# Performance work log

Measured on AMD Instinct MI355X. Metric: run time of the kernel, lower is better.

The kernel has to match this reference:

```python
import jax, jax.numpy as jnp
import numpy as np

B, S, H, NH, L, MLP_MULT = 4, 1024, 1024, 16, 2, 4
DK = H // NH
EPS = 1e-5


def setup_inputs() -> dict:
    key = jax.random.key(0)
    ks = jax.random.split(key, 8)
    p = lambda k, shape: jax.random.normal(k, shape, dtype=jnp.float32) * 0.02
    return {
        'hidden_states': jax.random.normal(ks[0], (B, S, H), dtype=jnp.float32),
        'attn_w': p(ks[1], (L, H, 3 * H)),
        'attn_b': jnp.zeros((L, 3 * H), jnp.float32),
        'proj_w': p(ks[2], (L, H, H)),
        'proj_b': jnp.zeros((L, H), jnp.float32),
        'fc_w': p(ks[3], (L, H, MLP_MULT * H)),
        'fc_b': jnp.zeros((L, MLP_MULT * H), jnp.float32),
        'fc2_w': p(ks[4], (L, MLP_MULT * H, H)),
        'fc2_b': jnp.zeros((L, H), jnp.float32),
        'ln1_g': jnp.ones((L, H), jnp.float32),
        'ln1_b': jnp.zeros((L, H), jnp.float32),
        'ln2_g': jnp.ones((L, H), jnp.float32),
        'ln2_b': jnp.zeros((L, H), jnp.float32),
        'position_ids': jnp.arange(S, dtype=jnp.int32),
    }


def _ln(x, g, b):
    m = jnp.mean(x, axis=-1, keepdims=True)
    v = jnp.var(x, axis=-1, keepdims=True)
    return (x - m) * jax.lax.rsqrt(v + EPS) * g + b


def _rotate_half(x):
    x1, x2 = jnp.split(x, 2, axis=-1)
    return jnp.concatenate((-x2, x1), axis=-1)


def _forward(hidden_states, attn_w, attn_b, proj_w, proj_b, fc_w, fc_b,
             fc2_w, fc2_b, ln1_g, ln1_b, ln2_g, ln2_b, position_ids):
    # rotary tables (fp32 math, as in RotaryEmbedding.forward)
    inv_freq = 1.0 / (10000.0 ** (jnp.arange(0, DK, 2, dtype=jnp.float32) / DK))
    freqs = position_ids.astype(jnp.float32)[:, None] * inv_freq[None, :]  # [S, DK/2]
    emb = jnp.concatenate((freqs, freqs), axis=-1)                          # [S, DK]
    cos = jnp.cos(emb)[None, None]  # [1,1,S,DK]
    sin = jnp.sin(emb)[None, None]
    causal = jnp.tril(jnp.ones((S, S), dtype=bool))
    neg = jnp.finfo(jnp.float32).min
    scale = 1.0 / np.sqrt(DK).astype(np.float32)

    h = hidden_states
    for i in range(L):
        # attention block
        x = _ln(h, ln1_g[i], ln1_b[i])
        qkv = x @ attn_w[i] + attn_b[i]                  # Conv1D c_attn
        q, k, v = jnp.split(qkv, 3, axis=-1)
        heads = lambda t: t.reshape(B, S, NH, DK).transpose(0, 2, 1, 3)
        q, k, v = heads(q), heads(k), heads(v)           # [B,NH,S,DK]
        q = q * cos + _rotate_half(q) * sin
        k = k * cos + _rotate_half(k) * sin
        # fp32 QK^T (baddbmm with alpha=scale, beta=0)
        w = jnp.einsum('bhqd,bhkd->bhqk', q.astype(jnp.float32),
                       k.astype(jnp.float32)) * scale    # [B,NH,S,S]
        w = jnp.where(causal, w, neg)
        w = jax.nn.softmax(w, axis=-1).astype(v.dtype)   # attn dropout is identity (eval)
        a = jnp.einsum('bhqk,bhkd->bhqd', w, v)
        a = a.transpose(0, 2, 1, 3).reshape(B, S, H)     # merge_heads
        h = h + (a @ proj_w[i] + proj_b[i])              # c_proj + residual
        # MLP block (gelu_new == tanh-approx gelu)
        x = _ln(h, ln2_g[i], ln2_b[i])
        mid = jax.nn.gelu(x @ fc_w[i] + fc_b[i], approximate=True)
        h = h + (mid @ fc2_w[i] + fc2_b[i])
    return h


def reference(hidden_states, attn_w, attn_b, proj_w, proj_b, fc_w, fc_b,
              fc2_w, fc2_b, ln1_g, ln1_b, ln2_g, ln2_b, position_ids):
    return _forward(hidden_states, attn_w, attn_b, proj_w, proj_b, fc_w, fc_b,
                    fc2_w, fc2_b, ln1_g, ln1_b, ln2_g, ln2_b, position_ids)
```

## Files before the change

kernel.cpp:

```cpp
#include <hip/hip_runtime.h>

#define B_ 4
#define S_ 1024
#define H_ 1024
#define NH_ 16
#define DK_ 64
#define MLPH_ 4096
#define EPS_ 1e-5f

typedef __attribute__((ext_vector_type(8))) short short8_t;
typedef __attribute__((ext_vector_type(8))) unsigned short ushort8_t;
typedef __attribute__((ext_vector_type(4))) float f32x4;

__device__ __forceinline__ unsigned short f2bf(float f) {
  unsigned int u = __float_as_uint(f);
  u = u + 0x7fffu + ((u >> 16) & 1u);
  return (unsigned short)(u >> 16);
}
__device__ __forceinline__ float bf2f(unsigned short b) {
  return __uint_as_float(((unsigned int)b) << 16);
}

__device__ __forceinline__ void gload16(const void* g, void* l) {
  typedef const __attribute__((address_space(1))) unsigned int GU;
  typedef __attribute__((address_space(3))) unsigned int LU;
  __builtin_amdgcn_global_load_lds((GU*)(size_t)g, (LU*)(unsigned int)(size_t)l, 16, 0, 0);
}

__device__ __forceinline__ float gelu_tanh(float x) {
  float y = 1.5957691216057308f * (x + 0.044715f * x * x * x);
  return x / (1.0f + __expf(-y));
}

__global__ __launch_bounds__(256) void wconv(const float* __restrict__ src0,
                                             unsigned short* __restrict__ dst0,
                                             int K, int N) {
  __shared__ float t[32][33];
  const float* src = src0 + (size_t)blockIdx.z * K * N;
  unsigned short* dst = dst0 + (size_t)blockIdx.z * N * K;
  int n0 = blockIdx.x * 32, k0 = blockIdx.y * 32;
  int tid = threadIdx.x;
  int r = tid >> 3, c = (tid & 7) * 4;
  const float* s = src + (size_t)(k0 + r) * N + n0 + c;
  float4 v = *(const float4*)s;
  t[r][c] = v.x; t[r][c + 1] = v.y; t[r][c + 2] = v.z; t[r][c + 3] = v.w;
  __syncthreads();
  ushort4 o;
  o.x = f2bf(t[c + 0][r]); o.y = f2bf(t[c + 1][r]);
  o.z = f2bf(t[c + 2][r]); o.w = f2bf(t[c + 3][r]);
  *(ushort4*)(dst + (size_t)(n0 + r) * K + k0 + c) = o;
}

__global__ __launch_bounds__(256) void ln_kernel(const float* __restrict__ x,
                                                 const float* __restrict__ g,
                                                 const float* __restrict__ b,
                                                 unsigned short* __restrict__ y) {
  int row = blockIdx.x, tid = threadIdx.x;
  const float* xp = x + (size_t)row * H_;
  float4 v = *((const float4*)xp + tid);
  float s  = v.x + v.y + v.z + v.w;
  float s2 = v.x * v.x + v.y * v.y + v.z * v.z + v.w * v.w;
  #pragma unroll
  for (int o = 1; o < 64; o <<= 1) {
    s  += __shfl_xor(s, o, 64);
    s2 += __shfl_xor(s2, o, 64);
  }
  __shared__ float r1[4], r2[4];
  if ((tid & 63) == 0) { r1[tid >> 6] = s; r2[tid >> 6] = s2; }
  __syncthreads();
  s  = r1[0] + r1[1] + r1[2] + r1[3];
  s2 = r2[0] + r2[1] + r2[2] + r2[3];
  float mean = s * (1.0f / H_);
  float var  = s2 * (1.0f / H_) - mean * mean;
  float inv  = rsqrtf(var + EPS_);
  float4 gv = *((const float4*)g + tid);
  float4 bv = *((const float4*)b + tid);
  ushort4 o;
  o.x = f2bf((v.x - mean) * inv * gv.x + bv.x);
  o.y = f2bf((v.y - mean) * inv * gv.y + bv.y);
  o.z = f2bf((v.z - mean) * inv * gv.z + bv.z);
  o.w = f2bf((v.w - mean) * inv * gv.w + bv.w);
  *(ushort4*)(y + (size_t)row * H_ + tid * 4) = o;
}

template <int MODE, int NT>
__global__ __launch_bounds__(256) void gemm_mfma(
    const unsigned short* __restrict__ A, const unsigned short* __restrict__ Bt,
    const float* __restrict__ bias, const float* __restrict__ resid,
    void* __restrict__ outp, int M, int N, int K, const int* __restrict__ pos) {
  constexpr int BN = NT * 32;
  constexpr int CB = BN / 32;
  __shared__ __align__(16) unsigned short As[2][128 * 64];
  __shared__ __align__(16) unsigned short Bs[2][BN * 64];
  int tid = threadIdx.x;
  int w = tid >> 6, lane = tid & 63;
  int gx = gridDim.x;
  int nwg = gx * gridDim.y;
  int bid = blockIdx.y * gx + blockIdx.x;
  int cpx = nwg >> 3;
  int swz = (bid & 7) * cpx + (bid >> 3);
  int m0 = (swz / gx) * 128, n0 = (swz % gx) * BN;
  int wr = w >> 1, wc = w & 1;
  int fr = lane & 15, kg = lane >> 4;
  f32x4 acc[4][NT];
  #pragma unroll
  for (int m = 0; m < 4; m++)
    #pragma unroll
    for (int n = 0; n < NT; n++) {
      acc[m][n][0] = 0.f; acc[m][n][1] = 0.f; acc[m][n][2] = 0.f; acc[m][n][3] = 0.f;
    }
  int srow = lane >> 3;
  int scol = ((lane & 7) ^ srow) * 8;
  const unsigned short* Ap = A  + (size_t)(m0 + w * 32 + srow) * K + scol;
  const unsigned short* Bp = Bt + (size_t)(n0 + w * (8 * CB) + srow) * K + scol;
  int sx = (fr & 7);
  int nk = K >> 6;
  {
    char* AsB = (char*)As[0] + w * 4096;
    char* BsB = (char*)Bs[0] + w * CB * 1024;
    #pragma unroll
    for (int i = 0; i < 4; i++) gload16(Ap + (size_t)i * 8 * K, AsB + i * 1024);
    #pragma unroll
    for (int i = 0; i < CB; i++) gload16(Bp + (size_t)i * 8 * K, BsB + i * 1024);
  }
  __syncthreads();
  for (int t = 0; t < nk; t++) {
    int cur = t & 1;
    if (t + 1 < nk) {
      const unsigned short* Ap2 = Ap + (size_t)(t + 1) * 64;
      const unsigned short* Bp2 = Bp + (size_t)(t + 1) * 64;
      char* AsB = (char*)As[cur ^ 1] + w * 4096;
      char* BsB = (char*)Bs[cur ^ 1] + w * CB * 1024;
      #pragma unroll
      for (int i = 0; i < 4; i++) gload16(Ap2 + (size_t)i * 8 * K, AsB + i * 1024);
      #pragma unroll
      for (int i = 0; i < CB; i++) gload16(Bp2 + (size_t)i * 8 * K, BsB + i * 1024);
    }
    #pragma unroll
    for (int kk = 0; kk < 2; kk++) {
      int slot = ((kk * 4 + kg) ^ sx) << 4;
      short8_t af[4], bfr[NT];
      #pragma unroll
      for (int m = 0; m < 4; m++)
        af[m] = *(const short8_t*)((char*)As[cur] + (wr * 64 + m * 16 + fr) * 128 + slot);
      #pragma unroll
      for (int n = 0; n < NT; n++)
        bfr[n] = *(const short8_t*)((char*)Bs[cur] + (wc * (NT * 16) + n * 16 + fr) * 128 + slot);
      #pragma unroll
      for (int m = 0; m < 4; m++)
        #pragma unroll
        for (int n = 0; n < NT; n++)
          acc[m][n] = __builtin_amdgcn_mfma_f32_16x16x32_bf16(af[m], bfr[n], acc[m][n], 0, 0, 0);
    }
    __syncthreads();
  }

  if (MODE == 3) {
    int seg = n0 >> 10;
    if (seg < 2) {
      #pragma unroll
      for (int n = 0; n < 2; n++) {
        int col0 = n0 + wc * 64 + n * 16 + fr;
        int d2 = n * 16 + fr;
        float invf = __expf(-0.2878231366242557f * (float)d2);
        float bv0 = bias[col0], bv2 = bias[col0 + 32];
        #pragma unroll
        for (int m = 0; m < 4; m++) {
          int row = m0 + wr * 64 + m * 16 + kg * 4;
          #pragma unroll
          for (int r = 0; r < 4; r++) {
            int s = (row + r) & (S_ - 1);
            float th = (float)pos[s] * invf;
            float sn, cs;
            __sincosf(th, &sn, &cs);
            float a0 = acc[m][n][r] + bv0;
            float a2 = acc[m][n + 2][r] + bv2;
            size_t base = (size_t)(row + r) * N;
            ((unsigned short*)outp)[base + col0]      = f2bf(a0 * cs - a2 * sn);
            ((unsigned short*)outp)[base + col0 + 32] = f2bf(a2 * cs + a0 * sn);
          }
        }
      }
    } else {
      #pragma unroll
      for (int n = 0; n < NT; n++) {
        int col = n0 + wc * (NT * 16) + n * 16 + fr;
        float bv = bias[col];
        #pragma unroll
        for (int m = 0; m < 4; m++) {
          int row = m0 + wr * 64 + m * 16 + kg * 4;
          #pragma unroll
          for (int r = 0; r < 4; r++)
            ((unsigned short*)outp)[(size_t)(row + r) * N + col] = f2bf(acc[m][n][r] + bv);
        }
      }
    }
    return;
  }
  #pragma unroll
  for (int n = 0; n < NT; n++) {
    int col = n0 + wc * (NT * 16) + n * 16 + fr;
    float bv = bias[col];
    #pragma unroll
    for (int m = 0; m < 4; m++) {
      int row = m0 + wr * 64 + m * 16 + kg * 4;
      #pragma unroll
      for (int r = 0; r < 4; r++) {
        float v = acc[m][n][r] + bv;
        size_t idx = (size_t)(row + r) * N + col;
        if (MODE == 2)      ((float*)outp)[idx] = resid[idx] + v;
        else if (MODE == 1) ((unsigned short*)outp)[idx] = f2bf(gelu_tanh(v));
        else                ((unsigned short*)outp)[idx] = f2bf(v);
      }
    }
  }
}

__global__ __launch_bounds__(256) void attn9(const unsigned short* __restrict__ qkv,
                                             unsigned short* __restrict__ aout) {
  __shared__ __align__(16) unsigned short Ks[2][64 * 64];
  __shared__ __align__(16) unsigned short Vt[2][64 * 64];
  __shared__ __align__(16) unsigned short Ps[4][16 * 64];
  const float SCL2 = 0.18033688011112443f;
  const float THR2 = 11.541560327111708f;
  int tid = threadIdx.x;
  int w = tid >> 6, lane = tid & 63;
  int fr = lane & 15, kg = lane >> 4;
  int lid = ((blockIdx.z << 4) + blockIdx.y) * 16 + blockIdx.x;
  int phase = lid >> 8, s256 = lid & 255;
  int i = s256 >> 6, combo = s256 & 63;
  int qt;
  if (phase == 0)      qt = 15 - i;
  else if (phase == 1) qt = i;
  else if (phase == 2) qt = 11 - i;
  else                 qt = 4 + i;
  int head = combo & 15, b = combo >> 4;
  int q0 = qt * 64;
  const unsigned short* base = qkv + ((size_t)b * S_) * 3072 + head * 64;

  const unsigned short* qp = base + (size_t)(q0 + w * 16 + fr) * 3072 + kg * 8;
  short8_t qa0 = *(const short8_t*)qp;
  short8_t qa1 = *(const short8_t*)(qp + 32);

  f32x4 acc[4];
  float mrun = -3.0e38f, lrun = 0.f;
  #pragma unroll
  for (int n = 0; n < 4; n++) {
    acc[n][0] = 0.f; acc[n][1] = 0.f; acc[n][2] = 0.f; acc[n][3] = 0.f;
  }

  int skv = lane;
  int sd0 = w * 16;
  int qrow = q0 + w * 16 + fr;

  const unsigned short* kp0 = base + 1024 + (size_t)skv * 3072 + sd0;
  short8_t ka = *(const short8_t*)kp0;
  short8_t kb = *(const short8_t*)(kp0 + 8);
  short8_t va = *(const short8_t*)(kp0 + 1024);
  short8_t vb = *(const short8_t*)(kp0 + 1032);

  int ntiles = qt + 1;
  for (int t = 0; t < ntiles; t++) {
    int cur = t & 1;
    {
      unsigned kbyte = skv * 128 + sd0 * 2;
      unsigned ksw = (skv & 7) << 4;
      *(short8_t*)((char*)Ks[cur] + (kbyte ^ ksw)) = ka;
      *(short8_t*)((char*)Ks[cur] + ((kbyte + 16) ^ ksw)) = kb;
      #pragma unroll
      for (int j = 0; j < 8; j++) {
        int d0 = sd0 + j, d1 = sd0 + 8 + j;
        *(unsigned short*)((char*)Vt[cur] + ((d0 * 128 + skv * 2) ^ ((d0 & 7) << 4))) = (unsigned short)va[j];
        *(unsigned short*)((char*)Vt[cur] + ((d1 * 128 + skv * 2) ^ ((d1 & 7) << 4))) = (unsigned short)vb[j];
      }
    }
    if (t + 1 < ntiles) {
      const unsigned short* kp = base + 1024 + (size_t)((t + 1) * 64 + skv) * 3072 + sd0;
      ka = *(const short8_t*)kp;
      kb = *(const short8_t*)(kp + 8);
      va = *(const short8_t*)(kp + 1024);
      vb = *(const short8_t*)(kp + 1032);
    }
    __syncthreads();
    short8_t b0[4], b1[4], v0[4], v1[4];
    #pragma unroll
    for (int n = 0; n < 4; n++) {
      int kvrow = n * 16 + fr;
      unsigned sw = (kvrow & 7) << 4;
      b0[n] = *(const short8_t*)((char*)Ks[cur] + ((kvrow * 128 + kg * 16) ^ sw));
      b1[n] = *(const short8_t*)((char*)Ks[cur] + ((kvrow * 128 + 64 + kg * 16) ^ sw));
    }
    #pragma unroll
    for (int n = 0; n < 4; n++) {
      int d = n * 16 + fr;
      unsigned sw = (d & 7) << 4;
      v0[n] = *(const short8_t*)((char*)Vt[cur] + ((d * 128 + kg * 16) ^ sw));
      v1[n] = *(const short8_t*)((char*)Vt[cur] + ((d * 128 + 64 + kg * 16) ^ sw));
    }
    f32x4 st[4];
    __builtin_amdgcn_s_setprio(1);
    #pragma unroll
    for (int n = 0; n < 4; n++) {
      f32x4 z; z[0] = 0.f; z[1] = 0.f; z[2] = 0.f; z[3] = 0.f;
      z = __builtin_amdgcn_mfma_f32_16x16x32_bf16(b0[n], qa0, z, 0, 0, 0);
      z = __builtin_amdgcn_mfma_f32_16x16x32_bf16(b1[n], qa1, z, 0, 0, 0);
      st[n] = z;
    }
    __builtin_amdgcn_s_setprio(0);
    bool diag = (t == qt);
    float rm = -3.0e38f;
    #pragma unroll
    for (int n = 0; n < 4; n++)
      #pragma unroll
      for (int j = 0; j < 4; j++) {
        float sv = st[n][j] * SCL2;
        if (diag && (t * 64 + n * 16 + kg * 4 + j > qrow)) sv = -1.0e30f;
        st[n][j] = sv;
        rm = fmaxf(rm, sv);
      }
    if (__any(rm > mrun + THR2)) {
      rm = fmaxf(rm, __shfl_xor(rm, 16, 64));
      rm = fmaxf(rm, __shfl_xor(rm, 32, 64));
      float mn = fmaxf(mrun, rm);
      float sc = exp2f(mrun - mn);
      mrun = mn;
      lrun *= sc;
      #pragma unroll
      for (int n = 0; n < 4; n++) {
        acc[n][0] *= sc; acc[n][1] *= sc; acc[n][2] *= sc; acc[n][3] *= sc;
      }
    }
    {
      float ls = 0.f;
      #pragma unroll
      for (int n = 0; n < 4; n++) {
        float e0 = exp2f(st[n][0] - mrun);
        float e1 = exp2f(st[n][1] - mrun);
        float e2 = exp2f(st[n][2] - mrun);
        float e3 = exp2f(st[n][3] - mrun);
        ls += (e0 + e1) + (e2 + e3);
        unsigned lo, hi;
        asm("v_cvt_pk_bf16_f32 %0, %1, %2" : "=v"(lo) : "v"(e0), "v"(e1));
        asm("v_cvt_pk_bf16_f32 %0, %1, %2" : "=v"(hi) : "v"(e2), "v"(e3));
        uint2 pk; pk.x = lo; pk.y = hi;
        *(uint2*)((char*)Ps[w] + ((fr * 128 + n * 32 + kg * 8) ^ ((fr & 7) << 4))) = pk;
      }
      lrun += ls;
    }
    asm volatile("s_waitcnt lgkmcnt(0)" ::: "memory");
    unsigned psw = (fr & 7) << 4;
    short8_t pa0 = *(const short8_t*)((char*)Ps[w] + ((fr * 128 + kg * 16) ^ psw));
    short8_t pa1 = *(const short8_t*)((char*)Ps[w] + ((fr * 128 + 64 + kg * 16) ^ psw));
    __builtin_amdgcn_s_setprio(1);
    #pragma unroll
    for (int n = 0; n < 4; n++) {
      acc[n] = __builtin_amdgcn_mfma_f32_16x16x32_bf16(v0[n], pa0, acc[n], 0, 0, 0);
      acc[n] = __builtin_amdgcn_mfma_f32_16x16x32_bf16(v1[n], pa1, acc[n], 0, 0, 0);
    }
    __builtin_amdgcn_s_setprio(0);
  }
  {
    float ls = lrun;
    ls += __shfl_xor(ls, 16, 64);
    ls += __shfl_xor(ls, 32, 64);
    float inv = 1.0f / ls;
    size_t row = (size_t)b * S_ + q0 + w * 16 + fr;
    unsigned short* op = aout + row * H_ + head * 64 + kg * 4;
    #pragma unroll
    for (int n = 0; n < 4; n++) {
      ushort4 o;
      o.x = f2bf(acc[n][0] * inv);
      o.y = f2bf(acc[n][1] * inv);
      o.z = f2bf(acc[n][2] * inv);
      o.w = f2bf(acc[n][3] * inv);
      *(ushort4*)(op + n * 16) = o;
    }
  }
}

extern "C" void kernel_launch(void* const* d_in, const int* in_sizes, int n_in,
                              void* d_out, int out_size, void* d_ws, size_t ws_size,
                              hipStream_t stream) {
  const float* hs     = (const float*)d_in[0];
  const float* attn_w = (const float*)d_in[1];
  const float* attn_b = (const float*)d_in[2];
  const float* proj_w = (const float*)d_in[3];
  const float* proj_b = (const float*)d_in[4];
  const float* fc_w   = (const float*)d_in[5];
  const float* fc_b   = (const float*)d_in[6];
  const float* fc2_w  = (const float*)d_in[7];
  const float* fc2_b  = (const float*)d_in[8];
  const float* ln1_g  = (const float*)d_in[9];
  const float* ln1_b  = (const float*)d_in[10];
  const float* ln2_g  = (const float*)d_in[11];
  const float* ln2_b  = (const float*)d_in[12];
  const int*   pos    = (const int*)d_in[13];

  float* hres = (float*)d_out;
  const size_t rows = (size_t)B_ * S_;

  unsigned short* wQ    = (unsigned short*)d_ws;
  unsigned short* wP    = wQ  + (size_t)2 * 3072 * 1024;
  unsigned short* wF1   = wP  + (size_t)2 * 1024 * 1024;
  unsigned short* wF2   = wF1 + (size_t)2 * 4096 * 1024;
  unsigned short* xbf   = wF2 + (size_t)2 * 1024 * 4096;
  unsigned short* qkvbf = xbf + rows * H_;
  unsigned short* midbf = qkvbf + rows * 3 * H_;
  unsigned short* aoutbf= midbf + rows * MLPH_;

  wconv<<<dim3(96, 32, 2), 256, 0, stream>>>(attn_w, wQ, 1024, 3072);
  wconv<<<dim3(32, 32, 2), 256, 0, stream>>>(proj_w, wP, 1024, 1024);
  wconv<<<dim3(128, 32, 2), 256, 0, stream>>>(fc_w, wF1, 1024, 4096);
  wconv<<<dim3(32, 128, 2), 256, 0, stream>>>(fc2_w, wF2, 4096, 1024);

  for (int l = 0; l < 2; l++) {
    const float* hin = (l == 0) ? hs : hres;
    ln_kernel<<<rows, 256, 0, stream>>>(hin, ln1_g + l * H_, ln1_b + l * H_, xbf);
    gemm_mfma<3, 4><<<dim3(24, 32), 256, 0, stream>>>(
        xbf, wQ + (size_t)l * 3072 * 1024, attn_b + (size_t)l * 3072, nullptr,
        qkvbf, 4096, 3072, 1024, pos);
    attn9<<<dim3(16, 16, 4), 256, 0, stream>>>(qkvbf, aoutbf);
    gemm_mfma<2, 2><<<dim3(16, 32), 256, 0, stream>>>(
        aoutbf, wP + (size_t)l * 1024 * 1024, proj_b + (size_t)l * 1024, hin,
        hres, 4096, 1024, 1024, nullptr);
    ln_kernel<<<rows, 256, 0, stream>>>(hres, ln2_g + l * H_, ln2_b + l * H_, xbf);
    gemm_mfma<1, 4><<<dim3(32, 32), 256, 0, stream>>>(
        xbf, wF1 + (size_t)l * 4096 * 1024, fc_b + (size_t)l * 4096, nullptr,
        midbf, 4096, 4096, 1024, nullptr);
    gemm_mfma<2, 2><<<dim3(16, 32), 256, 0, stream>>>(
        midbf, wF2 + (size_t)l * 1024 * 4096, fc2_b + (size_t)l * 1024, hres,
        hres, 4096, 1024, 4096, nullptr);
  }
}
```

Baseline: 406.6 us.

## Precompute rotary cos/sin table and remap GEMM tiles per XCD into 2D blocks

Adds a small kernel that builds a cos/sin table per position and frequency once, so the QKV GEMM epilogue reads float2 values instead of computing exp and sincos per element. It also changes the workgroup-to-tile mapping so each XCD (bid&7) covers a contiguous 2D region (quarter of rows, half of columns). That region is meant to improve L2 reuse of the A and B tiles within each XCD. It adds a table read in the epilogue and assumes gridDim.x is even and gridDim.y divisible by 4.

```diff
diff --git a/kernel.cpp b/kernel.cpp
--- a/kernel.cpp
+++ b/kernel.cpp
@@ -30,6 +30,17 @@
 __device__ __forceinline__ float gelu_tanh(float x) {
   float y = 1.5957691216057308f * (x + 0.044715f * x * x * x);
   return x / (1.0f + __expf(-y));
+}
+
+__global__ __launch_bounds__(256) void rope_tab_init(const int* __restrict__ pos,
+                                                     float2* __restrict__ tab) {
+  int idx = blockIdx.x * 256 + threadIdx.x;
+  int d2 = idx & 31, s = idx >> 5;
+  float invf = __expf(-0.2878231366242557f * (float)d2);
+  float th = (float)pos[s] * invf;
+  float sn, cs;
+  __sincosf(th, &sn, &cs);
+  tab[idx] = make_float2(cs, sn);
 }
 
 __global__ __launch_bounds__(256) void wconv(const float* __restrict__ src0,
@@ -87,7 +98,7 @@
 __global__ __launch_bounds__(256) void gemm_mfma(
     const unsigned short* __restrict__ A, const unsigned short* __restrict__ Bt,
     const float* __restrict__ bias, const float* __restrict__ resid,
-    void* __restrict__ outp, int M, int N, int K, const int* __restrict__ pos) {
+    void* __restrict__ outp, int M, int N, int K, const float2* __restrict__ rtab) {
   constexpr int BN = NT * 32;
   constexpr int CB = BN / 32;
   __shared__ __align__(16) unsigned short As[2][128 * 64];
@@ -95,11 +106,13 @@
   int tid = threadIdx.x;
   int w = tid >> 6, lane = tid & 63;
   int gx = gridDim.x;
-  int nwg = gx * gridDim.y;
   int bid = blockIdx.y * gx + blockIdx.x;
-  int cpx = nwg >> 3;
-  int swz = (bid & 7) * cpx + (bid >> 3);
-  int m0 = (swz / gx) * 128, n0 = (swz % gx) * BN;
+  int xcd = bid & 7, r = bid >> 3;
+  int rw = gx >> 1;
+  int ry = xcd >> 1, rx = xcd & 1;
+  int lm = r / rw, ln = r % rw;
+  int m0 = (ry * (gridDim.y >> 2) + lm) * 128;
+  int n0 = (rx * rw + ln) * BN;
   int wr = w >> 1, wc = w & 1;
   int fr = lane & 15, kg = lane >> 4;
   f32x4 acc[4][NT];
@@ -162,22 +175,19 @@
       for (int n = 0; n < 2; n++) {
         int col0 = n0 + wc * 64 + n * 16 + fr;
         int d2 = n * 16 + fr;
-        float invf = __expf(-0.2878231366242557f * (float)d2);
         float bv0 = bias[col0], bv2 = bias[col0 + 32];
         #pragma unroll
         for (int m = 0; m < 4; m++) {
           int row = m0 + wr * 64 + m * 16 + kg * 4;
           #pragma unroll
-          for (int r = 0; r < 4; r++) {
-            int s = (row + r) & (S_ - 1);
-            float th = (float)pos[s] * invf;
-            float sn, cs;
-            __sincosf(th, &sn, &cs);
-            float a0 = acc[m][n][r] + bv0;
-            float a2 = acc[m][n + 2][r] + bv2;
-            size_t base = (size_t)(row + r) * N;
-            ((unsigned short*)outp)[base + col0]      = f2bf(a0 * cs - a2 * sn);
-            ((unsigned short*)outp)[base + col0 + 32] = f2bf(a2 * cs + a0 * sn);
+          for (int r2 = 0; r2 < 4; r2++) {
+            int s = (row + r2) & (S_ - 1);
+            float2 cssn = rtab[(s << 5) + d2];
+            float a0 = acc[m][n][r2] + bv0;
+            float a2 = acc[m][n + 2][r2] + bv2;
+            size_t base = (size_t)(row + r2) * N;
+            ((unsigned short*)outp)[base + col0]      = f2bf(a0 * cssn.x - a2 * cssn.y);
+            ((unsigned short*)outp)[base + col0 + 32] = f2bf(a2 * cssn.x + a0 * cssn.y);
           }
         }
       }
@@ -190,8 +200,8 @@
         for (int m = 0; m < 4; m++) {
           int row = m0 + wr * 64 + m * 16 + kg * 4;
           #pragma unroll
-          for (int r = 0; r < 4; r++)
-            ((unsigned short*)outp)[(size_t)(row + r) * N + col] = f2bf(acc[m][n][r] + bv);
+          for (int r2 = 0; r2 < 4; r2++)
+            ((unsigned short*)outp)[(size_t)(row + r2) * N + col] = f2bf(acc[m][n][r2] + bv);
         }
       }
     }
@@ -205,9 +215,9 @@
     for (int m = 0; m < 4; m++) {
       int row = m0 + wr * 64 + m * 16 + kg * 4;
       #pragma unroll
-      for (int r = 0; r < 4; r++) {
-        float v = acc[m][n][r] + bv;
-        size_t idx = (size_t)(row + r) * N + col;
+      for (int r2 = 0; r2 < 4; r2++) {
+        float v = acc[m][n][r2] + bv;
+        size_t idx = (size_t)(row + r2) * N + col;
         if (MODE == 2)      ((float*)outp)[idx] = resid[idx] + v;
         else if (MODE == 1) ((unsigned short*)outp)[idx] = f2bf(gelu_tanh(v));
         else                ((unsigned short*)outp)[idx] = f2bf(v);
@@ -407,7 +417,9 @@
   unsigned short* qkvbf = xbf + rows * H_;
   unsigned short* midbf = qkvbf + rows * 3 * H_;
   unsigned short* aoutbf= midbf + rows * MLPH_;
-
+  float2* rtab = (float2*)(aoutbf + rows * H_);
+
+  rope_tab_init<<<128, 256, 0, stream>>>(pos, rtab);
   wconv<<<dim3(96, 32, 2), 256, 0, stream>>>(attn_w, wQ, 1024, 3072);
   wconv<<<dim3(32, 32, 2), 256, 0, stream>>>(proj_w, wP, 1024, 1024);
   wconv<<<dim3(128, 32, 2), 256, 0, stream>>>(fc_w, wF1, 1024, 4096);
@@ -418,7 +430,7 @@
     ln_kernel<<<rows, 256, 0, stream>>>(hin, ln1_g + l * H_, ln1_b + l * H_, xbf);
     gemm_mfma<3, 4><<<dim3(24, 32), 256, 0, stream>>>(
         xbf, wQ + (size_t)l * 3072 * 1024, attn_b + (size_t)l * 3072, nullptr,
-        qkvbf, 4096, 3072, 1024, pos);
+        qkvbf, 4096, 3072, 1024, rtab);
     attn9<<<dim3(16, 16, 4), 256, 0, stream>>>(qkvbf, aoutbf);
     gemm_mfma<2, 2><<<dim3(16, 32), 256, 0, stream>>>(
         aoutbf, wP + (size_t)l * 1024 * 1024, proj_b + (size_t)l * 1024, hin,
```

After: 405.4 us (median of 2 runs). Within noise of the previous version (-0.3%).
